# Optimization experiments

Hardware: AMD Instinct MI355X
Metric: run time of the kernel (lower is better)

Reference implementation:

```python
import jax, jax.numpy as jnp
import numpy as np

T = 2048      # sequence length (single unbatched sequence)
V = 32000     # vocab
D = 1024      # d_model
E = 16        # number of experts (one structural group)
TOPK = 2      # router top-k
CAP = 256     # per-expert capacity (T*TOPK/E)
DFF = 2048    # expert MLP hidden
NHOPS = 2     # number of routing hops
EPS = 1e-5    # RMSNorm eps


def setup_inputs() -> dict:
    key = jax.random.key(0)
    ks = jax.random.split(key, 6)
    ids = jax.random.randint(ks[0], (T,), 0, V)
    embed_W = jax.random.normal(ks[1], (V, D), jnp.float32) * 0.02
    ln_scale = jnp.ones((D,), jnp.float32)
    router_W = jax.random.normal(ks[2], (NHOPS, D, E), jnp.float32) * (D ** -0.5)
    expert_W1 = jax.random.normal(ks[3], (NHOPS, E, D, DFF), jnp.float32) * (D ** -0.5)
    expert_W2 = jax.random.normal(ks[4], (NHOPS, E, DFF, D), jnp.float32) * (DFF ** -0.5)
    return dict(ids=ids, embed_W=embed_W, ln_scale=ln_scale,
                router_W=router_W, expert_W1=expert_W1, expert_W2=expert_W2)


def _hop(h, Wr, W1, W2):
    # Router: clean logits -> mixing probs (softmax) + hard top-k selection mask.
    logits = h @ Wr                                   # (T, E)
    probs = jax.nn.softmax(logits, axis=-1)           # (T, E)
    _, top = jax.lax.top_k(logits, TOPK)              # (T, TOPK)
    mask = jnp.zeros((T, E), bool).at[jnp.arange(T)[:, None], top].set(True)

    # _capacity_select: rank tokens per expert by clean logits, keep top CAP.
    m = mask.T                                        # (E, T)
    g = jnp.where(m, logits.T, -jnp.inf)              # (E, T)
    _, top_idx = jax.lax.top_k(g, CAP)                # (E, C)
    slot = jnp.zeros((E, CAP, T), h.dtype)
    slot = slot.at[jnp.arange(E)[:, None], jnp.arange(CAP)[None, :], top_idx].set(1.0)
    slot = slot * m[:, None, :].astype(h.dtype)       # zero slots filled from -inf
    kept = slot.sum(1) > 0                            # (E, T)

    # One-hot einsum gather of token states into expert slot buffers.
    xin = jnp.einsum('ect,td->ecd', slot, h)          # (E, C, D)

    # Stable sort slots by original token position (active slots first).
    active = slot.sum(-1) > 0                         # (E, C)
    pos = jnp.where(active, top_idx, T + 1)
    order = jnp.argsort(pos, axis=1, stable=True)     # (E, C)
    xin = jnp.take_along_axis(xin, order[:, :, None], axis=1)
    slot = jnp.take_along_axis(slot, order[:, :, None], axis=1)

    # Grouped (stacked/vmapped) expert execution: GELU MLP per expert.
    h1 = jax.nn.gelu(jnp.einsum('ecd,edf->ecf', xin, W1))
    expert_out = jnp.einsum('ecf,efd->ecd', h1, W2)   # (E, C, D)

    # Combine (Eq. 3): h_{s+1} = h_s + sum_e rho_e (M_e(h) - h)
    cw = jnp.where(kept.T, probs, 0.0)                # (T, E)
    rho = cw.sum(axis=1, keepdims=True)               # (T, 1)
    combine = jnp.einsum('ecd,ect,et->td', expert_out, slot, cw.T)
    return h + combine - rho * h


def reference(ids, embed_W, ln_scale, router_W, expert_W1, expert_W2):
    h = embed_W[ids]                                  # (T, D) embedding lookup
    for i in range(NHOPS):
        h = _hop(h, router_W[i], expert_W1[i], expert_W2[i])
    # RMSNorm + tied unembedding
    h = h * jax.lax.rsqrt(jnp.mean(h * h, axis=-1, keepdims=True) + EPS) * ln_scale
    return h @ embed_W.T                              # (T, V)
```

## Files before the change

### kernel.cpp

```cpp
#include <hip/hip_runtime.h>
#include <stdint.h>

#define T_ 2048
#define V_ 32000
#define D_ 1024
#define E_ 16
#define CAP_ 256
#define DFF_ 2048

typedef unsigned short u16;
typedef unsigned int u32;
typedef __bf16 bf16x8 __attribute__((ext_vector_type(8)));
typedef float f32x4 __attribute__((ext_vector_type(4)));

__device__ __forceinline__ u16 f2bf(float f){
  u32 u = __float_as_uint(f);
  u32 r = u + 0x7FFFu + ((u >> 16) & 1u);
  return (u16)(r >> 16);
}
__device__ __forceinline__ float bf2f(u16 s){ return __uint_as_float(((u32)s) << 16); }

__device__ __forceinline__ void gl_lds16(const void* g, void* l){
  __builtin_amdgcn_global_load_lds((const __attribute__((address_space(1))) void*)g,
                                   (__attribute__((address_space(3))) void*)l, 16, 0, 0);
}
__device__ __forceinline__ f32x4 mfma16(bf16x8 a, bf16x8 b, f32x4 c){
  return __builtin_amdgcn_mfma_f32_16x16x32_bf16(a, b, c, 0, 0, 0);
}
__device__ __forceinline__ float gelu_tanh(float x){
  float u = 0.7978845608028654f * (x + 0.044715f * x * x * x);
  return 0.5f * x * (1.0f + tanhf(u));
}

__global__ __launch_bounds__(256) void k_cvtw(const float* __restrict__ W, u16* __restrict__ Wb){
  size_t i = ((size_t)blockIdx.x*256 + threadIdx.x)*8;
  float4 a = *(const float4*)(W + i);
  float4 b = *(const float4*)(W + i + 4);
  union { u16 s[8]; uint4 v; } p;
  p.s[0]=f2bf(a.x); p.s[1]=f2bf(a.y); p.s[2]=f2bf(a.z); p.s[3]=f2bf(a.w);
  p.s[4]=f2bf(b.x); p.s[5]=f2bf(b.y); p.s[6]=f2bf(b.z); p.s[7]=f2bf(b.w);
  *(uint4*)(Wb + i) = p.v;
}

template<bool EMB>
__global__ __launch_bounds__(256) void k_router(float* __restrict__ h,
    const float* __restrict__ Wr, float* __restrict__ logits,
    unsigned char* __restrict__ mask, int* __restrict__ top2, float* __restrict__ p2,
    const int* __restrict__ ids, const float* __restrict__ embW, int* __restrict__ etok){
  if (blockIdx.x < (E_*CAP_)/256) etok[blockIdx.x*256 + threadIdx.x] = -1;
  int w = threadIdx.x >> 6, l = threadIdx.x & 63;
  int t = blockIdx.x*4 + w;
  float acc[E_];
  #pragma unroll
  for (int e=0;e<E_;++e) acc[e]=0.f;
  const float* hrow = EMB ? (embW + (size_t)ids[t]*D_) : (h + (size_t)t*D_);
  #pragma unroll
  for (int i=0;i<16;++i){
    int d = l + i*64;
    float hv = hrow[d];
    if (EMB) h[(size_t)t*D_ + d] = hv;
    const float4* wr = (const float4*)(Wr + d*E_);
    float4 w0=wr[0], w1=wr[1], w2=wr[2], w3=wr[3];
    acc[0]+=hv*w0.x; acc[1]+=hv*w0.y; acc[2]+=hv*w0.z; acc[3]+=hv*w0.w;
    acc[4]+=hv*w1.x; acc[5]+=hv*w1.y; acc[6]+=hv*w1.z; acc[7]+=hv*w1.w;
    acc[8]+=hv*w2.x; acc[9]+=hv*w2.y; acc[10]+=hv*w2.z; acc[11]+=hv*w2.w;
    acc[12]+=hv*w3.x; acc[13]+=hv*w3.y; acc[14]+=hv*w3.z; acc[15]+=hv*w3.w;
  }
  #pragma unroll
  for (int off=32; off; off>>=1){
    #pragma unroll
    for (int e=0;e<E_;++e) acc[e] += __shfl_xor(acc[e], off, 64);
  }
  float mx = acc[0];
  #pragma unroll
  for (int e=1;e<E_;++e) mx = fmaxf(mx, acc[e]);
  float p[E_], s = 0.f;
  #pragma unroll
  for (int e=0;e<E_;++e){ p[e] = expf(acc[e]-mx); s += p[e]; }
  int i1 = 0; float v1 = acc[0];
  #pragma unroll
  for (int e=1;e<E_;++e) if (acc[e] > v1){ v1 = acc[e]; i1 = e; }
  int i2 = (i1==0)?1:0; float v2 = acc[i2];
  #pragma unroll
  for (int e=0;e<E_;++e) if (e!=i1 && e!=i2 && acc[e] > v2){ v2 = acc[e]; i2 = e; }
  if (l < E_){
    logits[t*E_+l] = acc[l];
    mask[t*E_+l] = (l==i1 || l==i2) ? 1 : 0;
  }
  if (l == 0){
    float inv = 1.f/s;
    top2[t*2] = i1; top2[t*2+1] = i2;
    p2[t*2] = p[i1]*inv; p2[t*2+1] = p[i2]*inv;
  }
}

__global__ __launch_bounds__(256) void k_capacity(const float* __restrict__ logits,
    const unsigned char* __restrict__ mask, const int* __restrict__ top2,
    int* __restrict__ kept, int* __restrict__ etok){
  int w = threadIdx.x >> 6, l = threadIdx.x & 63;
  int wid = blockIdx.x*4 + w;
  int t = wid >> 1, k = wid & 1;
  int e = top2[t*2+k];
  float my = logits[t*E_+e];
  int cnt = 0;
  for (int t2 = l; t2 < T_; t2 += 64){
    if (mask[t2*E_+e]){
      float lg = logits[t2*E_+e];
      if (lg > my || (lg == my && t2 < t)) cnt++;
    }
  }
  #pragma unroll
  for (int off=32; off; off>>=1) cnt += __shfl_xor(cnt, off, 64);
  if (l == 0){
    if (cnt < CAP_){ kept[t*2+k] = cnt; etok[e*CAP_+cnt] = t; }
    else kept[t*2+k] = -1;
  }
}

template<bool SPLIT>
__global__ __launch_bounds__(256) void k_gather(const float* __restrict__ h,
    const int* __restrict__ etok, u16* __restrict__ xhi, u16* __restrict__ xlo){
  int rc = blockIdx.x;
  int tok = etok[rc];
  int d = threadIdx.x * 4;
  float4 v = make_float4(0.f,0.f,0.f,0.f);
  if (tok >= 0) v = *(const float4*)(h + (size_t)tok*D_ + d);
  union { u16 s[4]; uint2 u; } hi, lo;
  hi.s[0]=f2bf(v.x); lo.s[0]=f2bf(v.x - bf2f(hi.s[0]));
  hi.s[1]=f2bf(v.y); lo.s[1]=f2bf(v.y - bf2f(hi.s[1]));
  hi.s[2]=f2bf(v.z); lo.s[2]=f2bf(v.z - bf2f(hi.s[2]));
  hi.s[3]=f2bf(v.w); lo.s[3]=f2bf(v.w - bf2f(hi.s[3]));
  *(uint2*)(xhi + (size_t)rc*D_ + d) = hi.u;
  if (SPLIT) *(uint2*)(xlo + (size_t)rc*D_ + d) = lo.u;
}

template<bool SPLIT, bool GELU, int BN>
__global__ __launch_bounds__(512, 1) void k_expert(
    const u16* __restrict__ Ahi, const u16* __restrict__ Alo,
    const float* __restrict__ Bw,
    u16* __restrict__ Ohi, u16* __restrict__ Olo, float* __restrict__ Of,
    int N, int K){
  constexpr int NI = BN/64;
  constexpr int ABYTES = 2*16384*(SPLIT?2:1);
  constexpr int BSLOT = BN*80;
  constexpr int BBYTES = 2*BSLOT*(SPLIT?2:1);
  __shared__ __align__(16) char sm[ABYTES + BBYTES];
  char* smA   = sm;
  char* smALo = sm + 32768;
  char* smB   = sm + ABYTES;
  char* smBLo = sm + ABYTES + 2*BSLOT;

  int bid = blockIdx.x;
  int swz = (bid & 7)*32 + (bid >> 3);
  int e  = swz >> 4;
  int n0 = (swz & 15) * BN;
  int tid = threadIdx.x;
  int lane = tid & 63;
  int w = tid >> 6;
  int wm = w >> 2, wn = w & 3;
  int lr = lane & 15, lq = lane >> 4;
  int NK = K >> 5;

  const u16* Ah = Ahi + (size_t)e*256*K;
  const u16* Al = SPLIT ? (Alo + (size_t)e*256*K) : (const u16*)nullptr;
  const float* Bb = Bw + (size_t)e*K*N + n0;

  f32x4 acc[8][NI];
  #pragma unroll
  for (int i=0;i<8;++i)
    #pragma unroll
    for (int j=0;j<NI;++j)
      #pragma unroll
      for (int c=0;c<4;++c) acc[i][j][c] = 0.f;

  int t2 = tid - 256;
  const u16* aSrcH[4]; const u16* aSrcL[4]; int aDst[4];
  #pragma unroll
  for (int r=0;r<4;++r){
    int o = r*4096 + t2*16;
    int row = o >> 6;
    int cs = ((o >> 4) & 3) ^ ((row >> 1) & 3);
    aDst[r] = o;
    aSrcH[r] = Ah + (size_t)row*K + cs*8;
    if (SPLIT) aSrcL[r] = Al + (size_t)row*K + cs*8;
  }
  int kb = (BN==128) ? (tid>>5) : (tid>>4);
  int nb = (BN==128) ? (tid&31) : (tid&15);
  int wOff[4];
  #pragma unroll
  for (int j=0;j<4;++j){
    int n = nb*4 + j;
    int pos;
    if (BN==128) pos = ((kb ^ (2*(nb&3))) & 7) * 8;
    else         pos = (kb*4) ^ ((nb&3)*16);
    wOff[j] = n*80 + pos;
  }
  float4 pb[4];

  #define LOADPB_(k0n) do { \
    if constexpr (BN==128){ \
      const float* bp = Bb + (size_t)((k0n) + kb*4)*N + nb*4; \
      pb[0] = *(const float4*)bp; pb[1] = *(const float4*)(bp + N); \
      pb[2] = *(const float4*)(bp + 2*N); pb[3] = *(const float4*)(bp + 3*N); \
    } else { \
      const float* bp = Bb + (size_t)((k0n) + kb*2)*N + nb*4; \
      pb[0] = *(const float4*)bp; pb[1] = *(const float4*)(bp + N); \
    } } while(0)

  #define WRITEB_(slot) do { \
    char* bh_ = smB + (slot)*BSLOT; char* bl_ = smBLo + (slot)*BSLOT; \
    if constexpr (BN==128){ \
      float cv[4][4] = {{pb[0].x,pb[1].x,pb[2].x,pb[3].x},{pb[0].y,pb[1].y,pb[2].y,pb[3].y}, \
                        {pb[0].z,pb[1].z,pb[2].z,pb[3].z},{pb[0].w,pb[1].w,pb[2].w,pb[3].w}}; \
      _Pragma("unroll") for (int j=0;j<4;++j){ \
        union { u16 s[4]; uint2 u; } hi, lo; \
        _Pragma("unroll") for (int i=0;i<4;++i){ \
          hi.s[i] = f2bf(cv[j][i]); \
          if constexpr (SPLIT) lo.s[i] = f2bf(cv[j][i] - bf2f(hi.s[i])); } \
        *(uint2*)(bh_ + wOff[j]) = hi.u; \
        if constexpr (SPLIT) *(uint2*)(bl_ + wOff[j]) = lo.u; } \
    } else { \
      float cv[4][2] = {{pb[0].x,pb[1].x},{pb[0].y,pb[1].y},{pb[0].z,pb[1].z},{pb[0].w,pb[1].w}}; \
      _Pragma("unroll") for (int j=0;j<4;++j){ \
        union { u16 s[2]; u32 u; } hi, lo; \
        _Pragma("unroll") for (int i=0;i<2;++i){ \
          hi.s[i] = f2bf(cv[j][i]); \
          if constexpr (SPLIT) lo.s[i] = f2bf(cv[j][i] - bf2f(hi.s[i])); } \
        *(u32*)(bh_ + wOff[j]) = hi.u; \
        if constexpr (SPLIT) *(u32*)(bl_ + wOff[j]) = lo.u; } \
    } } while(0)

  #define STAGEA_(k0n, slot) do { \
    _Pragma("unroll") for (int r=0;r<4;++r){ \
      gl_lds16(aSrcH[r] + (k0n), smA + (slot)*16384 + aDst[r]); \
      if constexpr (SPLIT) gl_lds16(aSrcL[r] + (k0n), smALo + (slot)*16384 + aDst[r]); \
    } } while(0)

  if (tid < 256){
    LOADPB_(0);
    WRITEB_(0);
    if (NK > 1) LOADPB_(32);
  } else {
    STAGEA_(0, 0);
  }
  __syncthreads();

  int aRo[8];
  #pragma unroll
  for (int mi=0;mi<8;++mi){
    int row = wm*128 + mi*16 + lr;
    aRo[mi] = row*64 + ((lq ^ ((row>>1)&3))<<4);
  }
  int bRo[NI];
  #pragma unroll
  for (int ni=0;ni<NI;++ni){
    int n = wn*(BN/4) + ni*16 + lr;
    bRo[ni] = n*80 + ((lq ^ ((n>>2)&3))<<4);
  }

  for (int ks = 0; ks < NK; ++ks){
    int cur = ks & 1;
    bf16x8 bh[NI], bl[NI];
    #pragma unroll
    for (int ni=0;ni<NI;++ni){
      bh[ni] = *(const bf16x8*)(smB + cur*BSLOT + bRo[ni]);
      if constexpr (SPLIT) bl[ni] = *(const bf16x8*)(smBLo + cur*BSLOT + bRo[ni]);
    }
    if (ks + 1 < NK){
      int nslot = cur ^ 1;
      if (tid < 256){
        WRITEB_(nslot);
        if (ks + 2 < NK) LOADPB_((ks+2)*32);
      } else {
        STAGEA_((ks+1)*32, nslot);
      }
    }
    #pragma unroll
    for (int mi=0;mi<8;++mi){
      bf16x8 ah = *(const bf16x8*)(smA + cur*16384 + aRo[mi]);
      if constexpr (SPLIT){
        bf16x8 al = *(const bf16x8*)(smALo + cur*16384 + aRo[mi]);
        #pragma unroll
        for (int ni=0;ni<NI;++ni){
          acc[mi][ni] = mfma16(ah, bh[ni], acc[mi][ni]);
          acc[mi][ni] = mfma16(al, bh[ni], acc[mi][ni]);
          acc[mi][ni] = mfma16(ah, bl[ni], acc[mi][ni]);
        }
      } else {
        #pragma unroll
        for (int ni=0;ni<NI;++ni)
          acc[mi][ni] = mfma16(ah, bh[ni], acc[mi][ni]);
      }
    }
    __syncthreads();
  }
  #undef LOADPB_
  #undef WRITEB_
  #undef STAGEA_

  {
    constexpr int STRIPB = NI*16*4*16;
    char* strip = sm + w*STRIPB;
    int r = lane & 15;
    int b = lane >> 4;
    #pragma unroll
    for (int mi=0;mi<8;++mi){
      #pragma unroll
      for (int ni=0;ni<NI;++ni){
        int col = ni*16 + lr;
        f32x4 v = acc[mi][ni];
        if constexpr (GELU){
          v[0]=gelu_tanh(v[0]); v[1]=gelu_tanh(v[1]);
          v[2]=gelu_tanh(v[2]); v[3]=gelu_tanh(v[3]);
        }
        *(f32x4*)(strip + (col*4 + lq)*16) = v;
      }
      asm volatile("s_waitcnt lgkmcnt(0)" ::: "memory");
      __builtin_amdgcn_sched_barrier(0);
      int grow = wm*128 + mi*16 + r;
      if constexpr (GELU){
        union { u16 s[8]; uint4 v; } ph, pl;
        #pragma unroll
        for (int i=0;i<8;++i){
          float y = *(const float*)(strip + ((b*8+i)*4 + (r>>2))*16 + (r&3)*4);
          ph.s[i] = f2bf(y);
          if constexpr (SPLIT) pl.s[i] = f2bf(y - bf2f(ph.s[i]));
        }
        size_t idx = ((size_t)e*256 + grow)*N + n0 + wn*(BN/4) + b*8;
        *(uint4*)(Ohi + idx) = ph.v;
        if constexpr (SPLIT) *(uint4*)(Olo + idx) = pl.v;
      } else {
        #pragma unroll
        for (int cc=0; cc<NI; ++cc){
          int c = b + cc*4;
          float4 o;
          o.x = *(const float*)(strip + ((c*4+0)*4 + (r>>2))*16 + (r&3)*4);
          o.y = *(const float*)(strip + ((c*4+1)*4 + (r>>2))*16 + (r&3)*4);
          o.z = *(const float*)(strip + ((c*4+2)*4 + (r>>2))*16 + (r&3)*4);
          o.w = *(const float*)(strip + ((c*4+3)*4 + (r>>2))*16 + (r&3)*4);
          *(float4*)(Of + ((size_t)e*256 + grow)*N + n0 + wn*(BN/4) + c*4) = o;
        }
      }
      asm volatile("s_waitcnt lgkmcnt(0)" ::: "memory");
    }
  }
}

template<bool FINAL>
__global__ __launch_bounds__(256) void k_combine(float* __restrict__ h,
    const float* __restrict__ Y2, const int* __restrict__ top2,
    const float* __restrict__ p2, const int* __restrict__ kept,
    const float* __restrict__ g, u16* __restrict__ hn){
  int t = blockIdx.x;
  int e0 = top2[t*2], e1 = top2[t*2+1];
  int r0 = kept[t*2], r1 = kept[t*2+1];
  float w0 = (r0 >= 0) ? p2[t*2]   : 0.f;
  float w1 = (r1 >= 0) ? p2[t*2+1] : 0.f;
  float om = 1.f - w0 - w1;
  int d = threadIdx.x * 4;
  float4 v = *(const float4*)(h + (size_t)t*D_ + d);
  float ox = v.x*om, oy = v.y*om, oz = v.z*om, ow = v.w*om;
  if (r0 >= 0){
    float4 y = *(const float4*)(Y2 + ((size_t)e0*CAP_ + r0)*D_ + d);
    ox += w0*y.x; oy += w0*y.y; oz += w0*y.z; ow += w0*y.w;
  }
  if (r1 >= 0){
    float4 y = *(const float4*)(Y2 + ((size_t)e1*CAP_ + r1)*D_ + d);
    ox += w1*y.x; oy += w1*y.y; oz += w1*y.z; ow += w1*y.w;
  }
  if constexpr (!FINAL){
    *(float4*)(h + (size_t)t*D_ + d) = make_float4(ox, oy, oz, ow);
  } else {
    int w = threadIdx.x >> 6, l = threadIdx.x & 63;
    __shared__ float red[4];
    float ss = ox*ox + oy*oy + oz*oz + ow*ow;
    #pragma unroll
    for (int off=32; off; off>>=1) ss += __shfl_xor(ss, off, 64);
    if (l == 0) red[w] = ss;
    __syncthreads();
    float tot = red[0] + red[1] + red[2] + red[3];
    float sc = rsqrtf(tot * (1.f/D_) + 1e-5f);
    float4 gs = *(const float4*)(g + d);
    union { u16 s[4]; uint2 u; } o;
    o.s[0] = f2bf(ox*sc*gs.x); o.s[1] = f2bf(oy*sc*gs.y);
    o.s[2] = f2bf(oz*sc*gs.z); o.s[3] = f2bf(ow*sc*gs.w);
    *(uint2*)(hn + (size_t)t*D_ + d) = o.u;
  }
}

#define SLOT_ 16384
__global__ __launch_bounds__(512, 2) void k_gemm_final(const u16* __restrict__ A,
    const u16* __restrict__ B, float* __restrict__ C){
  __shared__ __align__(16) char lds[131072];
  char* ldsA = lds;
  char* ldsB = lds + 65536;
  int bid = blockIdx.x;
  int wgid = (bid & 7) * 125 + (bid >> 3);
  int m0 = (wgid & 7) << 8;
  int n0 = (wgid >> 3) << 8;
  int tid = threadIdx.x;
  int lane = tid & 63;
  int w = tid >> 6;
  int wm = w >> 2, wn = w & 3;
  int lr = lane & 15, lq = lane >> 4;

  f32x4 acc[8][4];
  #pragma unroll
  for (int i=0;i<8;++i)
    #pragma unroll
    for (int j=0;j<4;++j)
      #pragma unroll
      for (int c=0;c<4;++c) acc[i][j][c] = 0.f;

  int j_0 = w*2, j_1 = w*2 + 1;
  int rp0 = j_0*8 + (lane>>3), rp1 = j_1*8 + (lane>>3);
  int c80 = (lane&7) ^ (rp0&7), c81 = (lane&7) ^ (rp1&7);
  int rA0 = rp0*2 + (c80>>2), rA1 = rp1*2 + (c81>>2);
  int cc0 = (c80&3)*8,        cc1 = (c81&3)*8;
  const u16* sA0 = A + (size_t)(m0+rA0)*D_ + cc0;
  const u16* sA1 = A + (size_t)(m0+rA1)*D_ + cc1;
  const u16* sB0 = B + (size_t)(n0+rA0)*D_ + cc0;
  const u16* sB1 = B + (size_t)(n0+rA1)*D_ + cc1;
  int d0 = j_0*1024 + lane*16, d1 = j_1*1024 + lane*16;

  int aoff[8], boff[4];
  #pragma unroll
  for (int mi=0;mi<8;++mi){
    int r = wm*128 + mi*16 + lr;
    int rp = r >> 1;
    int c8 = ((r&1)<<2) | lq;
    aoff[mi] = rp*128 + ((c8 ^ (rp&7))<<4);
  }
  #pragma unroll
  for (int ni=0;ni<4;++ni){
    int r = wn*64 + ni*16 + lr;
    int rp = r >> 1;
    int c8 = ((r&1)<<2) | lq;
    boff[ni] = rp*128 + ((c8 ^ (rp&7))<<4);
  }

  #define STAGE_(sbase) do { \
    gl_lds16(sA0, ldsA + (sbase) + d0); gl_lds16(sB0, ldsB + (sbase) + d0); \
    gl_lds16(sA1, ldsA + (sbase) + d1); gl_lds16(sB1, ldsB + (sbase) + d1); \
    sA0 += 32; sA1 += 32; sB0 += 32; sB1 += 32; } while(0)

  bf16x8 aF0[8], bF0[4], aF1[8], bF1[4];

  STAGE_(0); STAGE_(SLOT_); STAGE_(2*SLOT_);
  asm volatile("s_waitcnt vmcnt(8)" ::: "memory");
  __builtin_amdgcn_s_barrier();
  {
    const char* pA_ = ldsA; const char* pB_ = ldsB;
    #pragma unroll
    for (int ni=0;ni<4;++ni) bF0[ni] = *(const bf16x8*)(pB_ + boff[ni]);
    #pragma unroll
    for (int mi=0;mi<8;++mi) aF0[mi] = *(const bf16x8*)(pA_ + aoff[mi]);
  }

  #define PHASE_(kh, FAc, FBc, FAn, FBn) do { \
    if ((kh) <= 28) STAGE_((((kh)+3)&3)*SLOT_); \
    if ((kh) <= 28)      asm volatile("s_waitcnt vmcnt(8)" ::: "memory"); \
    else if ((kh) == 29) asm volatile("s_waitcnt vmcnt(4)" ::: "memory"); \
    else if ((kh) == 30) asm volatile("s_waitcnt vmcnt(0)" ::: "memory"); \
    asm volatile("s_waitcnt lgkmcnt(0)" ::: "memory"); \
    __builtin_amdgcn_sched_barrier(0); \
    __builtin_amdgcn_s_barrier(); \
    __builtin_amdgcn_sched_barrier(0); \
    if ((kh) < 31){ \
      int sb_ = (((kh)+1)&3)*SLOT_; \
      const char* pA_ = ldsA + sb_; const char* pB_ = ldsB + sb_; \
      _Pragma("unroll") for (int ni=0;ni<4;++ni) FBn[ni] = *(const bf16x8*)(pB_ + boff[ni]); \
      _Pragma("unroll") for (int mi=0;mi<8;++mi) FAn[mi] = *(const bf16x8*)(pA_ + aoff[mi]); \
    } \
    __builtin_amdgcn_s_setprio(1); \
    _Pragma("unroll") for (int mi=0;mi<8;++mi){ \
      _Pragma("unroll") for (int ni=0;ni<4;++ni) \
        acc[mi][ni] = mfma16(FAc[mi], FBc[ni], acc[mi][ni]); \
    } \
    __builtin_amdgcn_s_setprio(0); \
  } while(0)

  for (int kh2 = 0; kh2 < 32; kh2 += 2){
    PHASE_(kh2,     aF0, bF0, aF1, bF1);
    PHASE_(kh2 + 1, aF1, bF1, aF0, bF0);
  }
  #undef PHASE_
  #undef STAGE_

  {
    char* strip = lds + w*4096;
    int r = lane & 15;
    int b = lane >> 4;
    #pragma unroll
    for (int mi=0;mi<8;++mi){
      #pragma unroll
      for (int ni=0;ni<4;++ni){
        int col = ni*16 + lr;
        *(f32x4*)(strip + (col*4 + lq)*16) = acc[mi][ni];
      }
      asm volatile("s_waitcnt lgkmcnt(0)" ::: "memory");
      __builtin_amdgcn_sched_barrier(0);
      int grow = m0 + wm*128 + mi*16 + r;
      #pragma unroll
      for (int cc=0; cc<4; ++cc){
        int c = b + cc*4;
        float4 o;
        o.x = *(const float*)(strip + ((c*4+0)*4 + (r>>2))*16 + (r&3)*4);
        o.y = *(const float*)(strip + ((c*4+1)*4 + (r>>2))*16 + (r&3)*4);
        o.z = *(const float*)(strip + ((c*4+2)*4 + (r>>2))*16 + (r&3)*4);
        o.w = *(const float*)(strip + ((c*4+3)*4 + (r>>2))*16 + (r&3)*4);
        *(float4*)(&C[(size_t)grow*V_ + n0 + wn*64 + c*4]) = o;
      }
      asm volatile("s_waitcnt lgkmcnt(0)" ::: "memory");
    }
  }
}

extern "C" void kernel_launch(void* const* d_in, const int* in_sizes, int n_in,
                              void* d_out, int out_size, void* d_ws, size_t ws_size,
                              hipStream_t stream){
  const int*   ids  = (const int*)d_in[0];
  const float* embW = (const float*)d_in[1];
  const float* lns  = (const float*)d_in[2];
  const float* WrA  = (const float*)d_in[3];
  const float* W1A  = (const float*)d_in[4];
  const float* W2A  = (const float*)d_in[5];
  float* out = (float*)d_out;
  char* ws = (char*)d_ws;
  const size_t MB = 1u << 20;

  float* h      = (float*)(ws);
  float* logits = (float*)(ws + 8*MB);
  unsigned char* mask = (unsigned char*)(ws + 8*MB + 131072);
  int*   top2v  = (int*)(ws + 8*MB + 131072 + 32768);
  float* p2     = (float*)(ws + 8*MB + 131072 + 32768 + 16384);
  int*   kept   = (int*)(ws + 8*MB + 131072 + 32768 + 32768);
  int*   etok   = (int*)(ws + 8*MB + 131072 + 32768 + 49152);
  u16*   xhi  = (u16*)(ws + 9*MB);
  u16*   xlo  = (u16*)(ws + 17*MB);
  float* y2   = (float*)(ws + 9*MB);
  u16*   y1hi = (u16*)(ws + 25*MB);
  u16*   y1lo = (u16*)(ws + 41*MB);
  u16*   hn   = (u16*)(ws + 57*MB);
  u16*   ebf  = (u16*)(ws + 61*MB);

  k_cvtw<<<(V_*D_)/(256*8), 256, 0, stream>>>(embW, ebf);

  for (int hop = 0; hop < 2; ++hop){
    const float* Wr = WrA + (size_t)hop*D_*E_;
    const float* W1 = W1A + (size_t)hop*E_*D_*DFF_;
    const float* W2 = W2A + (size_t)hop*E_*DFF_*D_;
    if (hop == 0){
      k_router<true ><<<T_/4, 256, 0, stream>>>(h, Wr, logits, mask, top2v, p2, ids, embW, etok);
      k_capacity<<<T_*2/4, 256, 0, stream>>>(logits, mask, top2v, kept, etok);
      k_gather<true ><<<E_*CAP_, 256, 0, stream>>>(h, etok, xhi, xlo);
      k_expert<true , true , 128><<<E_*(DFF_/128), 512, 0, stream>>>(
          xhi, xlo, W1, y1hi, y1lo, nullptr, DFF_, D_);
      k_expert<true , false, 64 ><<<E_*(D_/64), 512, 0, stream>>>(
          y1hi, y1lo, W2, nullptr, nullptr, y2, D_, DFF_);
      k_combine<false><<<T_, 256, 0, stream>>>(h, y2, top2v, p2, kept, lns, hn);
    } else {
      k_router<false><<<T_/4, 256, 0, stream>>>(h, Wr, logits, mask, top2v, p2, ids, embW, etok);
      k_capacity<<<T_*2/4, 256, 0, stream>>>(logits, mask, top2v, kept, etok);
      k_gather<false><<<E_*CAP_, 256, 0, stream>>>(h, etok, xhi, xlo);
      k_expert<false, true , 128><<<E_*(DFF_/128), 512, 0, stream>>>(
          xhi, nullptr, W1, y1hi, nullptr, nullptr, DFF_, D_);
      k_expert<false, false, 64 ><<<E_*(D_/64), 512, 0, stream>>>(
          y1hi, nullptr, W2, nullptr, nullptr, y2, D_, DFF_);
      k_combine<true ><<<T_, 256, 0, stream>>>(h, y2, top2v, p2, kept, lns, hn);
    }
  }

  k_gemm_final<<<(T_/256)*(V_/256), 512, 0, stream>>>(hn, ebf, out);
}
```

Baseline: 642.2 us.

## Shrink final unembedding GEMM tile to 128x128 with 256-thread blocks

The final T×V GEMM moves from 256x256 tiles with 512 threads and 128 KB LDS to 128x128 tiles with 256 threads and 64 KB LDS, which quadruples the grid. It also adjusts the XCD-aware block swizzle and the LDS swizzle pattern. The LDS-transposed, float4-vectorized epilogue is replaced by direct scalar fp32 stores. The aim is better occupancy and load balance across CUs, at the cost of lower operand reuse per tile and less coalesced output writes for the large fp32 output.

```diff
diff --git a/kernel.cpp b/kernel.cpp
--- a/kernel.cpp
+++ b/kernel.cpp
@@ -388,77 +388,74 @@
   }
 }
 
-#define SLOT_ 16384
-__global__ __launch_bounds__(512, 2) void k_gemm_final(const u16* __restrict__ A,
+#define FSLOT_ 8192
+__global__ __launch_bounds__(256, 2) void k_gemm_final(const u16* __restrict__ A,
     const u16* __restrict__ B, float* __restrict__ C){
-  __shared__ __align__(16) char lds[131072];
+  __shared__ __align__(16) char lds[65536];
   char* ldsA = lds;
-  char* ldsB = lds + 65536;
+  char* ldsB = lds + 32768;
   int bid = blockIdx.x;
-  int wgid = (bid & 7) * 125 + (bid >> 3);
-  int m0 = (wgid & 7) << 8;
-  int n0 = (wgid >> 3) << 8;
+  int swz = (bid & 7)*500 + (bid >> 3);
+  int m0 = (swz & 15) << 7;
+  int n0 = (swz >> 4) << 7;
   int tid = threadIdx.x;
   int lane = tid & 63;
   int w = tid >> 6;
-  int wm = w >> 2, wn = w & 3;
+  int wm = w >> 1, wn = w & 1;
   int lr = lane & 15, lq = lane >> 4;
 
-  f32x4 acc[8][4];
-  #pragma unroll
-  for (int i=0;i<8;++i)
+  f32x4 acc[4][4];
+  #pragma unroll
+  for (int i=0;i<4;++i)
     #pragma unroll
     for (int j=0;j<4;++j)
       #pragma unroll
       for (int c=0;c<4;++c) acc[i][j][c] = 0.f;
 
-  int j_0 = w*2, j_1 = w*2 + 1;
-  int rp0 = j_0*8 + (lane>>3), rp1 = j_1*8 + (lane>>3);
-  int c80 = (lane&7) ^ (rp0&7), c81 = (lane&7) ^ (rp1&7);
-  int rA0 = rp0*2 + (c80>>2), rA1 = rp1*2 + (c81>>2);
-  int cc0 = (c80&3)*8,        cc1 = (c81&3)*8;
-  const u16* sA0 = A + (size_t)(m0+rA0)*D_ + cc0;
-  const u16* sA1 = A + (size_t)(m0+rA1)*D_ + cc1;
-  const u16* sB0 = B + (size_t)(n0+rA0)*D_ + cc0;
-  const u16* sB1 = B + (size_t)(n0+rA1)*D_ + cc1;
-  int d0 = j_0*1024 + lane*16, d1 = j_1*1024 + lane*16;
-
-  int aoff[8], boff[4];
-  #pragma unroll
-  for (int mi=0;mi<8;++mi){
-    int r = wm*128 + mi*16 + lr;
-    int rp = r >> 1;
-    int c8 = ((r&1)<<2) | lq;
-    aoff[mi] = rp*128 + ((c8 ^ (rp&7))<<4);
+  int row0 = w*32 + (lane >> 2);
+  int row1 = row0 + 16;
+  int c = lane & 3;
+  int cs0 = c ^ ((row0 >> 1) & 3);
+  int cs1 = c ^ ((row1 >> 1) & 3);
+  const u16* sA0 = A + (size_t)(m0+row0)*D_ + cs0*8;
+  const u16* sA1 = A + (size_t)(m0+row1)*D_ + cs1*8;
+  const u16* sB0 = B + (size_t)(n0+row0)*D_ + cs0*8;
+  const u16* sB1 = B + (size_t)(n0+row1)*D_ + cs1*8;
+  int d0 = w*2048 + lane*16;
+  int d1 = d0 + 1024;
+
+  int aoff[4], boff[4];
+  #pragma unroll
+  for (int mi=0;mi<4;++mi){
+    int r = wm*64 + mi*16 + lr;
+    aoff[mi] = r*64 + ((lq ^ ((r>>1)&3))<<4);
   }
   #pragma unroll
   for (int ni=0;ni<4;++ni){
     int r = wn*64 + ni*16 + lr;
-    int rp = r >> 1;
-    int c8 = ((r&1)<<2) | lq;
-    boff[ni] = rp*128 + ((c8 ^ (rp&7))<<4);
-  }
-
-  #define STAGE_(sbase) do { \
-    gl_lds16(sA0, ldsA + (sbase) + d0); gl_lds16(sB0, ldsB + (sbase) + d0); \
-    gl_lds16(sA1, ldsA + (sbase) + d1); gl_lds16(sB1, ldsB + (sbase) + d1); \
+    boff[ni] = r*64 + ((lq ^ ((r>>1)&3))<<4);
+  }
+
+  #define STAGE_(slot) do { \
+    gl_lds16(sA0, ldsA + (slot)*FSLOT_ + d0); gl_lds16(sB0, ldsB + (slot)*FSLOT_ + d0); \
+    gl_lds16(sA1, ldsA + (slot)*FSLOT_ + d1); gl_lds16(sB1, ldsB + (slot)*FSLOT_ + d1); \
     sA0 += 32; sA1 += 32; sB0 += 32; sB1 += 32; } while(0)
 
-  bf16x8 aF0[8], bF0[4], aF1[8], bF1[4];
-
-  STAGE_(0); STAGE_(SLOT_); STAGE_(2*SLOT_);
+  #define READF_(slot, FA, FB) do { \
+    const char* pA_ = ldsA + (slot)*FSLOT_; const char* pB_ = ldsB + (slot)*FSLOT_; \
+    _Pragma("unroll") for (int ni=0;ni<4;++ni) FB[ni] = *(const bf16x8*)(pB_ + boff[ni]); \
+    _Pragma("unroll") for (int mi=0;mi<4;++mi) FA[mi] = *(const bf16x8*)(pA_ + aoff[mi]); \
+  } while(0)
+
+  bf16x8 aF0[4], bF0[4], aF1[4], bF1[4];
+
+  STAGE_(0); STAGE_(1); STAGE_(2);
   asm volatile("s_waitcnt vmcnt(8)" ::: "memory");
   __builtin_amdgcn_s_barrier();
-  {
-    const char* pA_ = ldsA; const char* pB_ = ldsB;
-    #pragma unroll
-    for (int ni=0;ni<4;++ni) bF0[ni] = *(const bf16x8*)(pB_ + boff[ni]);
-    #pragma unroll
-    for (int mi=0;mi<8;++mi) aF0[mi] = *(const bf16x8*)(pA_ + aoff[mi]);
-  }
+  READF_(0, aF0, bF0);
 
   #define PHASE_(kh, FAc, FBc, FAn, FBn) do { \
-    if ((kh) <= 28) STAGE_((((kh)+3)&3)*SLOT_); \
+    if ((kh) <= 28) STAGE_(((kh)+3)&3); \
     if ((kh) <= 28)      asm volatile("s_waitcnt vmcnt(8)" ::: "memory"); \
     else if ((kh) == 29) asm volatile("s_waitcnt vmcnt(4)" ::: "memory"); \
     else if ((kh) == 30) asm volatile("s_waitcnt vmcnt(0)" ::: "memory"); \
@@ -466,14 +463,9 @@
     __builtin_amdgcn_sched_barrier(0); \
     __builtin_amdgcn_s_barrier(); \
     __builtin_amdgcn_sched_barrier(0); \
-    if ((kh) < 31){ \
-      int sb_ = (((kh)+1)&3)*SLOT_; \
-      const char* pA_ = ldsA + sb_; const char* pB_ = ldsB + sb_; \
-      _Pragma("unroll") for (int ni=0;ni<4;++ni) FBn[ni] = *(const bf16x8*)(pB_ + boff[ni]); \
-      _Pragma("unroll") for (int mi=0;mi<8;++mi) FAn[mi] = *(const bf16x8*)(pA_ + aoff[mi]); \
-    } \
+    if ((kh) < 31) READF_(((kh)+1)&3, FAn, FBn); \
     __builtin_amdgcn_s_setprio(1); \
-    _Pragma("unroll") for (int mi=0;mi<8;++mi){ \
+    _Pragma("unroll") for (int mi=0;mi<4;++mi){ \
       _Pragma("unroll") for (int ni=0;ni<4;++ni) \
         acc[mi][ni] = mfma16(FAc[mi], FBc[ni], acc[mi][ni]); \
     } \
@@ -485,35 +477,19 @@
     PHASE_(kh2 + 1, aF1, bF1, aF0, bF0);
   }
   #undef PHASE_
+  #undef READF_
   #undef STAGE_
 
-  {
-    char* strip = lds + w*4096;
-    int r = lane & 15;
-    int b = lane >> 4;
-    #pragma unroll
-    for (int mi=0;mi<8;++mi){
+  #pragma unroll
+  for (int mi=0;mi<4;++mi)
+    #pragma unroll
+    for (int ni=0;ni<4;++ni)
       #pragma unroll
-      for (int ni=0;ni<4;++ni){
-        int col = ni*16 + lr;
-        *(f32x4*)(strip + (col*4 + lq)*16) = acc[mi][ni];
+      for (int j=0;j<4;++j){
+        int row = m0 + wm*64 + mi*16 + lq*4 + j;
+        int col = n0 + wn*64 + ni*16 + lr;
+        C[(size_t)row * V_ + col] = acc[mi][ni][j];
       }
-      asm volatile("s_waitcnt lgkmcnt(0)" ::: "memory");
-      __builtin_amdgcn_sched_barrier(0);
-      int grow = m0 + wm*128 + mi*16 + r;
-      #pragma unroll
-      for (int cc=0; cc<4; ++cc){
-        int c = b + cc*4;
-        float4 o;
-        o.x = *(const float*)(strip + ((c*4+0)*4 + (r>>2))*16 + (r&3)*4);
-        o.y = *(const float*)(strip + ((c*4+1)*4 + (r>>2))*16 + (r&3)*4);
-        o.z = *(const float*)(strip + ((c*4+2)*4 + (r>>2))*16 + (r&3)*4);
-        o.w = *(const float*)(strip + ((c*4+3)*4 + (r>>2))*16 + (r&3)*4);
-        *(float4*)(&C[(size_t)grow*V_ + n0 + wn*64 + c*4]) = o;
-      }
-      asm volatile("s_waitcnt lgkmcnt(0)" ::: "memory");
-    }
-  }
 }
 
 extern "C" void kernel_launch(void* const* d_in, const int* in_sizes, int n_in,
@@ -571,5 +547,5 @@
     }
   }
 
-  k_gemm_final<<<(T_/256)*(V_/256), 512, 0, stream>>>(hn, ebf, out);
-}
+  k_gemm_final<<<(T_/128)*(V_/128), 256, 0, stream>>>(hn, ebf, out);
+}
```

Result: slower. 690.6 us (+7.5%).
